# Performance work log

Hardware: AMD Instinct MI355X
Metric: run time of the kernel (lower is better)

The kernel has to match this reference:

```python
import jax, jax.numpy as jnp
import numpy as np

N = 100000        # nodes in the batched graph
E = 1_600_000     # directed edges
G = 256           # graphs in the batch
IN, H = 3, 64
EPS = 1e-5        # BatchNorm eps (eval mode: running stats, dropout off)


def setup_inputs() -> dict:
    key = jax.random.key(0)
    ks = jax.random.split(key, 40)
    inp = {}
    inp["x"] = jax.random.normal(ks[0], (N, IN), jnp.float32)
    inp["edge_index"] = jax.random.randint(ks[1], (2, E), 0, N, dtype=jnp.int32)
    inp["batch_idx"] = jnp.sort(jax.random.randint(ks[2], (N,), 0, G, dtype=jnp.int32))
    dims = [IN, H, H, H]  # zip(dims[:-1], dims[1:]) -> 3 GCN layers (as in source)
    k = 3
    for i in range(3):
        inp[f"W{i}"] = jax.random.normal(ks[k], (dims[i], dims[i + 1]), jnp.float32) * 0.1; k += 1
        inp[f"b{i}"] = jax.random.normal(ks[k], (dims[i + 1],), jnp.float32) * 0.01; k += 1
        inp[f"g{i}"] = jax.random.uniform(ks[k], (dims[i + 1],), jnp.float32, 0.5, 1.5); k += 1
        inp[f"be{i}"] = jax.random.normal(ks[k], (dims[i + 1],), jnp.float32) * 0.1; k += 1
        inp[f"rm{i}"] = jax.random.normal(ks[k], (dims[i + 1],), jnp.float32) * 0.1; k += 1
        inp[f"rv{i}"] = jax.random.uniform(ks[k], (dims[i + 1],), jnp.float32, 0.5, 1.5); k += 1
    inp["mW1"] = jax.random.normal(ks[k], (2 * H, 32), jnp.float32) * 0.1; k += 1
    inp["mb1"] = jnp.zeros((32,), jnp.float32)
    inp["mW2"] = jax.random.normal(ks[k], (32, 16), jnp.float32) * 0.1; k += 1
    inp["mb2"] = jnp.zeros((16,), jnp.float32)
    inp["mW3"] = jax.random.normal(ks[k], (16, 1), jnp.float32) * 0.1; k += 1
    inp["mb3"] = jnp.zeros((1,), jnp.float32)
    return inp


def _gcn(x, W, b, src, dst):
    # PyG GCNConv: add self-loops, symmetric D^-1/2 (A+I) D^-1/2 normalization
    h = x @ W                                   # [N, out]
    deg = jnp.zeros((N,), h.dtype).at[dst].add(1.0) + 1.0  # +1 self-loop
    dinv = jax.lax.rsqrt(deg)
    coef = dinv[src] * dinv[dst]                # [E]
    agg = jax.ops.segment_sum(h[src] * coef[:, None], dst, num_segments=N)
    agg = agg + h * (dinv * dinv)[:, None]      # self-loop message
    return agg + b


def _bn(x, g, be, rm, rv):
    return (x - rm) * jax.lax.rsqrt(rv + EPS) * g + be


def _forward(x, edge_index, batch_idx,
             W0, b0, g0, be0, rm0, rv0,
             W1, b1, g1, be1, rm1, rv1,
             W2, b2, g2, be2, rm2, rv2,
             mW1, mb1, mW2, mb2, mW3, mb3):
    src, dst = edge_index[0], edge_index[1]
    layers = [(W0, b0, g0, be0, rm0, rv0), (W1, b1, g1, be1, rm1, rv1), (W2, b2, g2, be2, rm2, rv2)]
    for (W, b, g, be, rm, rv) in layers:
        x = jax.nn.relu(_bn(_gcn(x, W, b, src, dst), g, be, rm, rv))
    cnt = jax.ops.segment_sum(jnp.ones((N,), x.dtype), batch_idx, num_segments=G)
    x_mean = jax.ops.segment_sum(x, batch_idx, num_segments=G) / jnp.maximum(cnt, 1.0)[:, None]
    x_max = jax.ops.segment_max(x, batch_idx, num_segments=G)
    x_max = jnp.where(jnp.isfinite(x_max), x_max, 0.0)
    xg = jnp.concatenate([x_mean, x_max], axis=1)  # [G, 2H]
    h = jax.nn.relu(xg @ mW1 + mb1)
    h = jax.nn.relu(h @ mW2 + mb2)
    return h @ mW3 + mb3                            # [G, 1]


def reference(x, edge_index, batch_idx,
              W0, b0, g0, be0, rm0, rv0,
              W1, b1, g1, be1, rm1, rv1,
              W2, b2, g2, be2, rm2, rv2,
              mW1, mb1, mW2, mb2, mW3, mb3):
    return _forward(x, edge_index, batch_idx,
                    W0, b0, g0, be0, rm0, rv0,
                    W1, b1, g1, be1, rm1, rv1,
                    W2, b2, g2, be2, rm2, rv2,
                    mW1, mb1, mW2, mb2, mW3, mb3)
```

## Files before the change

### kernel.cpp

```cpp
#include <hip/hip_runtime.h>
#include <hip/hip_fp16.h>

#define NN 100000
#define EE 1600000
#define GG 256
#define EPS 1e-5f
#define KB2 ((NN + 511) >> 9)
#define BCAP 10240
#define EPB 4096
#define EBLK ((EE + EPB - 1) / EPB)
#define NB256 ((NN + 255) / 256)

__device__ __forceinline__ unsigned int pack2(float x, float y) {
  __half2 h = __float22half2_rn(make_float2(x, y));
  return *reinterpret_cast<unsigned int*>(&h);
}
__device__ __forceinline__ uint2 pack4(float x, float y, float z, float w) {
  uint2 r;
  r.x = pack2(x, y);
  r.y = pack2(z, w);
  return r;
}
__device__ __forceinline__ void add8(float4& a0, float4& a1, uint4 v) {
  __half2 h0 = *reinterpret_cast<__half2*>(&v.x);
  __half2 h1 = *reinterpret_cast<__half2*>(&v.y);
  __half2 h2 = *reinterpret_cast<__half2*>(&v.z);
  __half2 h3 = *reinterpret_cast<__half2*>(&v.w);
  float2 f0 = __half22float2(h0), f1 = __half22float2(h1);
  float2 f2 = __half22float2(h2), f3 = __half22float2(h3);
  a0.x += f0.x; a0.y += f0.y; a0.z += f1.x; a0.w += f1.y;
  a1.x += f2.x; a1.y += f2.y; a1.z += f3.x; a1.w += f3.y;
}

__device__ __forceinline__ void gld16(uint4& d, const uint4* p) {
  asm volatile("global_load_dwordx4 %0, %1, off" : "=v"(d) : "v"(p));
}
__device__ __forceinline__ void gld4(int& d, const int* p) {
  asm volatile("global_load_dword %0, %1, off" : "=v"(d) : "v"(p));
}

__global__ void k_passA(const int* __restrict__ ei, int* __restrict__ bfill,
                        int* __restrict__ tmp) {
  __shared__ int cnt[KB2], cur[KB2], base[KB2];
  int t = threadIdx.x;
  for (int b = t; b < KB2; b += 256) { cnt[b] = 0; cur[b] = 0; }
  __syncthreads();
  int e0 = blockIdx.x * EPB;
  int myb[16];
#pragma unroll
  for (int j = 0; j < 16; ++j) {
    int e = e0 + j * 256 + t;
    int bb = -1;
    if (e < EE) bb = ei[EE + e] >> 9;
    myb[j] = bb;
    if (bb >= 0) atomicAdd(&cnt[bb], 1);
  }
  __syncthreads();
  for (int b = t; b < KB2; b += 256)
    if (cnt[b] > 0) base[b] = b * BCAP + atomicAdd(&bfill[b], cnt[b]);
  __syncthreads();
#pragma unroll
  for (int j = 0; j < 16; ++j) {
    int e = e0 + j * 256 + t;
    int bb = myb[j];
    if (bb >= 0) {
      int slot = base[bb] + atomicAdd(&cur[bb], 1);
      tmp[slot] = (ei[e] << 9) | (ei[EE + e] & 511);
    }
  }
}

__global__ void k_bucket(const int* __restrict__ tmp, const int* __restrict__ bfill,
                         const float* __restrict__ x, int* __restrict__ csr,
                         int* __restrict__ row, int* __restrict__ rowe,
                         float* __restrict__ dinv, float4* __restrict__ xd) {
  __shared__ int cnt[512], s[512], fillp[512];
  int b = blockIdx.x, t = threadIdx.x;
  int nb = b << 9;
  int e0 = b * BCAP, e1 = e0 + bfill[b];
  cnt[t] = 0;
  cnt[t + 256] = 0;
  __syncthreads();
  for (int e = e0 + t; e < e1; e += 256) atomicAdd(&cnt[tmp[e] & 511], 1);
  __syncthreads();
  s[t] = cnt[t];
  s[t + 256] = cnt[t + 256];
  __syncthreads();
  for (int off = 1; off < 512; off <<= 1) {
    int i1 = t + 256;
    int v0 = (t >= off) ? s[t - off] : 0;
    int v1 = (i1 >= off) ? s[i1 - off] : 0;
    __syncthreads();
    s[t] += v0;
    s[i1] += v1;
    __syncthreads();
  }
#pragma unroll
  for (int k = 0; k < 2; ++k) {
    int i = t + k * 256;
    int excl = s[i] - cnt[i];
    fillp[i] = excl;
    int dst = nb + i;
    if (dst < NN) {
      row[dst] = e0 + excl;
      rowe[dst] = e0 + s[i];
      float d = rsqrtf((float)cnt[i] + 1.0f);
      dinv[dst] = d;
      xd[dst] = make_float4(x[dst * 3] * d, x[dst * 3 + 1] * d, x[dst * 3 + 2] * d, 0.f);
    }
  }
  __syncthreads();
  for (int e = e0 + t; e < e1; e += 256) {
    int ed = tmp[e];
    int slot = atomicAdd(&fillp[ed & 511], 1);
    csr[e0 + slot] = ed >> 9;
  }
}

__global__ void k_agg3f(const float4* __restrict__ xd, const int* __restrict__ row,
                        const int* __restrict__ rowe, const int* __restrict__ csr,
                        const float* __restrict__ dinv,
                        const float* __restrict__ W, const float* __restrict__ b,
                        const float* __restrict__ gam, const float* __restrict__ bet,
                        const float* __restrict__ rm, const float* __restrict__ rv,
                        uint2* __restrict__ out) {
  int n = blockIdx.x * 256 + threadIdx.x;
  if (n >= NN) return;
  int s0 = row[n], s1 = rowe[n];
  float4 a = xd[n];
  float ax = a.x, ay = a.y, az = a.z;
  for (int i = s0; i < s1; i += 16) {
    int rem = s1 - i;
    int idx[16];
#pragma unroll
    for (int j = 0; j < 16; ++j) idx[j] = csr[min(i + j, s1 - 1)];
    float4 v[16];
#pragma unroll
    for (int j = 0; j < 16; ++j) v[j] = xd[idx[j]];
#pragma unroll
    for (int j = 0; j < 16; ++j)
      if (j < rem) { ax += v[j].x; ay += v[j].y; az += v[j].z; }
  }
  float d = dinv[n];
  float t0 = ax * d, t1 = ay * d, t2 = az * d;
  const float4* W4 = (const float4*)W;
  const float4* b4 = (const float4*)b;
  const float4* g4p = (const float4*)gam;
  const float4* be4p = (const float4*)bet;
  const float4* rm4p = (const float4*)rm;
  const float4* rv4p = (const float4*)rv;
#pragma unroll
  for (int c4 = 0; c4 < 16; ++c4) {
    float4 w0 = W4[c4], w1 = W4[16 + c4], w2 = W4[32 + c4];
    float4 bb = b4[c4], g4 = g4p[c4], be4 = be4p[c4], rm4 = rm4p[c4], rv4 = rv4p[c4];
    float4 o;
    o.x = fmaf(t0, w0.x, fmaf(t1, w1.x, fmaf(t2, w2.x, bb.x)));
    o.y = fmaf(t0, w0.y, fmaf(t1, w1.y, fmaf(t2, w2.y, bb.y)));
    o.z = fmaf(t0, w0.z, fmaf(t1, w1.z, fmaf(t2, w2.z, bb.z)));
    o.w = fmaf(t0, w0.w, fmaf(t1, w1.w, fmaf(t2, w2.w, bb.w)));
    float scx = g4.x * rsqrtf(rv4.x + EPS), shx = be4.x - rm4.x * scx;
    float scy = g4.y * rsqrtf(rv4.y + EPS), shy = be4.y - rm4.y * scy;
    float scz = g4.z * rsqrtf(rv4.z + EPS), shz = be4.z - rm4.z * scz;
    float scw = g4.w * rsqrtf(rv4.w + EPS), shw = be4.w - rm4.w * scw;
    o.x = fmaxf(fmaf(o.x, scx, shx), 0.f) * d;
    o.y = fmaxf(fmaf(o.y, scy, shy), 0.f) * d;
    o.z = fmaxf(fmaf(o.z, scz, shz), 0.f) * d;
    o.w = fmaxf(fmaf(o.w, scw, shw), 0.f) * d;
    out[(size_t)n * 16 + c4] = pack4(o.x, o.y, o.z, o.w);
  }
}

template <bool MID>
__launch_bounds__(256, 4)
__global__ void k_layer2(const uint4* __restrict__ xs, const int* __restrict__ row,
                         const int* __restrict__ rowe, const int* __restrict__ csr,
                         const float* __restrict__ dinv,
                         const float* __restrict__ W, const float* __restrict__ b,
                         const float* __restrict__ gam, const float* __restrict__ bet,
                         const float* __restrict__ rm, const float* __restrict__ rv,
                         void* __restrict__ outv) {
  __shared__ float sh[32][68];
  int t = blockIdx.x * 256 + threadIdx.x;
  int n = t >> 3, sub = t & 7;
  int local = threadIdx.x >> 3;
  int s0 = row[n], s1 = rowe[n];
  float4 a0 = make_float4(0.f, 0.f, 0.f, 0.f);
  float4 a1 = make_float4(0.f, 0.f, 0.f, 0.f);
  add8(a0, a1, xs[(size_t)n * 8 + sub]);
  if (s0 < s1) {
    int e = s0 + sub;
    int myidx = (e < s1) ? csr[e] : n;
    for (int i = s0; i < s1; i += 8) {
      int e2 = i + 8 + sub;
      int pre;
      gld4(pre, csr + min(e2, s1 - 1));
      uint4 v0, v1, v2, v3, v4, v5, v6, v7;
      gld16(v0, xs + ((size_t)__shfl(myidx, 0, 8) * 8 + sub));
      gld16(v1, xs + ((size_t)__shfl(myidx, 1, 8) * 8 + sub));
      gld16(v2, xs + ((size_t)__shfl(myidx, 2, 8) * 8 + sub));
      gld16(v3, xs + ((size_t)__shfl(myidx, 3, 8) * 8 + sub));
      gld16(v4, xs + ((size_t)__shfl(myidx, 4, 8) * 8 + sub));
      gld16(v5, xs + ((size_t)__shfl(myidx, 5, 8) * 8 + sub));
      gld16(v6, xs + ((size_t)__shfl(myidx, 6, 8) * 8 + sub));
      gld16(v7, xs + ((size_t)__shfl(myidx, 7, 8) * 8 + sub));
      asm volatile("s_waitcnt vmcnt(0)" ::: "memory");
      __builtin_amdgcn_sched_barrier(0);
      int rem = s1 - i;
      add8(a0, a1, v0);
      if (rem > 1) add8(a0, a1, v1);
      if (rem > 2) add8(a0, a1, v2);
      if (rem > 3) add8(a0, a1, v3);
      if (rem > 4) add8(a0, a1, v4);
      if (rem > 5) add8(a0, a1, v5);
      if (rem > 6) add8(a0, a1, v6);
      if (rem > 7) add8(a0, a1, v7);
      myidx = (e2 < s1) ? pre : n;
    }
  }
  float d = dinv[n];
  float4 w0 = make_float4(a0.x * d, a0.y * d, a0.z * d, a0.w * d);
  float4 w1 = make_float4(a1.x * d, a1.y * d, a1.z * d, a1.w * d);
  *(float4*)&sh[local][sub * 8] = w0;
  *(float4*)&sh[local][sub * 8 + 4] = w1;
  __syncthreads();
  const float4* W4 = (const float4*)W;
  float4 accA = ((const float4*)b)[sub * 2];
  float4 accB = ((const float4*)b)[sub * 2 + 1];
#pragma unroll 8
  for (int k = 0; k < 64; ++k) {
    float xv = sh[local][k];
    float4 wA = W4[k * 16 + sub * 2];
    float4 wB = W4[k * 16 + sub * 2 + 1];
    accA.x = fmaf(xv, wA.x, accA.x);
    accA.y = fmaf(xv, wA.y, accA.y);
    accA.z = fmaf(xv, wA.z, accA.z);
    accA.w = fmaf(xv, wA.w, accA.w);
    accB.x = fmaf(xv, wB.x, accB.x);
    accB.y = fmaf(xv, wB.y, accB.y);
    accB.z = fmaf(xv, wB.z, accB.z);
    accB.w = fmaf(xv, wB.w, accB.w);
  }
  float4 gA = ((const float4*)gam)[sub * 2], gB = ((const float4*)gam)[sub * 2 + 1];
  float4 beA = ((const float4*)bet)[sub * 2], beB = ((const float4*)bet)[sub * 2 + 1];
  float4 rmA = ((const float4*)rm)[sub * 2], rmB = ((const float4*)rm)[sub * 2 + 1];
  float4 rvA = ((const float4*)rv)[sub * 2], rvB = ((const float4*)rv)[sub * 2 + 1];
  float4 oA, oB;
  {
    float sc = gA.x * rsqrtf(rvA.x + EPS); oA.x = fmaxf(fmaf(accA.x, sc, beA.x - rmA.x * sc), 0.f);
    sc = gA.y * rsqrtf(rvA.y + EPS); oA.y = fmaxf(fmaf(accA.y, sc, beA.y - rmA.y * sc), 0.f);
    sc = gA.z * rsqrtf(rvA.z + EPS); oA.z = fmaxf(fmaf(accA.z, sc, beA.z - rmA.z * sc), 0.f);
    sc = gA.w * rsqrtf(rvA.w + EPS); oA.w = fmaxf(fmaf(accA.w, sc, beA.w - rmA.w * sc), 0.f);
    sc = gB.x * rsqrtf(rvB.x + EPS); oB.x = fmaxf(fmaf(accB.x, sc, beB.x - rmB.x * sc), 0.f);
    sc = gB.y * rsqrtf(rvB.y + EPS); oB.y = fmaxf(fmaf(accB.y, sc, beB.y - rmB.y * sc), 0.f);
    sc = gB.z * rsqrtf(rvB.z + EPS); oB.z = fmaxf(fmaf(accB.z, sc, beB.z - rmB.z * sc), 0.f);
    sc = gB.w * rsqrtf(rvB.w + EPS); oB.w = fmaxf(fmaf(accB.w, sc, beB.w - rmB.w * sc), 0.f);
  }
  if (MID) {
    uint4 r;
    r.x = pack2(oA.x * d, oA.y * d);
    r.y = pack2(oA.z * d, oA.w * d);
    r.z = pack2(oB.x * d, oB.y * d);
    r.w = pack2(oB.z * d, oB.w * d);
    ((uint4*)outv)[(size_t)n * 8 + sub] = r;
  } else {
    ((float4*)outv)[(size_t)n * 16 + sub * 2] = oA;
    ((float4*)outv)[(size_t)n * 16 + sub * 2 + 1] = oB;
  }
}

__device__ __forceinline__ int lower_bound(const int* __restrict__ b, int target) {
  int lo = 0, hi = NN;
  while (lo < hi) {
    int m = (lo + hi) >> 1;
    if (b[m] < target) lo = m + 1; else hi = m;
  }
  return lo;
}

__global__ void k_poolmlp(const float4* __restrict__ feat, const int* __restrict__ bidx,
                          const float* __restrict__ mW1, const float* __restrict__ mb1,
                          const float* __restrict__ mW2, const float* __restrict__ mb2,
                          const float* __restrict__ mW3, const float* __restrict__ mb3,
                          float* __restrict__ out) {
  __shared__ float4 shs[16][17], shm[16][17];
  __shared__ float xg[128], h1[32], h2[16];
  int g = blockIdx.x, t = threadIdx.x;
  int c4 = t & 15, r = t >> 4;
  int lo = lower_bound(bidx, g);
  int hi = lower_bound(bidx, g + 1);
  float4 s = make_float4(0.f, 0.f, 0.f, 0.f);
  float4 m = make_float4(0.f, 0.f, 0.f, 0.f);
  for (int i = lo + r; i < hi; i += 16) {
    float4 v = feat[(size_t)i * 16 + c4];
    s.x += v.x; s.y += v.y; s.z += v.z; s.w += v.w;
    m.x = fmaxf(m.x, v.x); m.y = fmaxf(m.y, v.y);
    m.z = fmaxf(m.z, v.z); m.w = fmaxf(m.w, v.w);
  }
  shs[r][c4] = s;
  shm[r][c4] = m;
  __syncthreads();
  if (t < 16) {
    float4 cs = shs[0][t], cm = shm[0][t];
#pragma unroll
    for (int r2 = 1; r2 < 16; ++r2) {
      float4 as = shs[r2][t], am = shm[r2][t];
      cs.x += as.x; cs.y += as.y; cs.z += as.z; cs.w += as.w;
      cm.x = fmaxf(cm.x, am.x); cm.y = fmaxf(cm.y, am.y);
      cm.z = fmaxf(cm.z, am.z); cm.w = fmaxf(cm.w, am.w);
    }
    float inv = 1.0f / fmaxf((float)(hi - lo), 1.0f);
    xg[t * 4 + 0] = cs.x * inv; xg[t * 4 + 1] = cs.y * inv;
    xg[t * 4 + 2] = cs.z * inv; xg[t * 4 + 3] = cs.w * inv;
    xg[64 + t * 4 + 0] = cm.x; xg[64 + t * 4 + 1] = cm.y;
    xg[64 + t * 4 + 2] = cm.z; xg[64 + t * 4 + 3] = cm.w;
  }
  __syncthreads();
  if (t < 32) {
    float a = mb1[t];
    for (int k = 0; k < 128; ++k) a = fmaf(xg[k], mW1[k * 32 + t], a);
    h1[t] = fmaxf(a, 0.f);
  }
  __syncthreads();
  if (t < 16) {
    float a = mb2[t];
    for (int k = 0; k < 32; ++k) a = fmaf(h1[k], mW2[k * 16 + t], a);
    h2[t] = fmaxf(a, 0.f);
  }
  __syncthreads();
  if (t == 0) {
    float a = mb3[0];
    for (int k = 0; k < 16; ++k) a = fmaf(h2[k], mW3[k], a);
    out[g] = a;
  }
}

extern "C" void kernel_launch(void* const* d_in, const int* in_sizes, int n_in,
                              void* d_out, int out_size, void* d_ws, size_t ws_size,
                              hipStream_t stream) {
  const float* x = (const float*)d_in[0];
  const int* ei = (const int*)d_in[1];
  const int* bidx = (const int*)d_in[2];
  const float *W[3], *b[3], *gam[3], *bet[3], *rm[3], *rv[3];
  for (int l = 0; l < 3; ++l) {
    W[l] = (const float*)d_in[3 + 6 * l];
    b[l] = (const float*)d_in[4 + 6 * l];
    gam[l] = (const float*)d_in[5 + 6 * l];
    bet[l] = (const float*)d_in[6 + 6 * l];
    rm[l] = (const float*)d_in[7 + 6 * l];
    rv[l] = (const float*)d_in[8 + 6 * l];
  }
  const float* mW1 = (const float*)d_in[21];
  const float* mb1 = (const float*)d_in[22];
  const float* mW2 = (const float*)d_in[23];
  const float* mb2 = (const float*)d_in[24];
  const float* mW3 = (const float*)d_in[25];
  const float* mb3 = (const float*)d_in[26];
  float* out = (float*)d_out;

  char* ws = (char*)d_ws;
  size_t off = 0;
  auto alloc = [&](size_t bytes) {
    void* p = ws + off;
    off = (off + bytes + 1023) & ~(size_t)1023;
    return p;
  };
  float* dinv = (float*)alloc(NN * 4);
  int* row = (int*)alloc(NN * 4);
  int* rowe = (int*)alloc(NN * 4);
  int* csr = (int*)alloc((size_t)KB2 * BCAP * 4);
  int* bfill = (int*)alloc(256 * 4);
  float4* xd = (float4*)alloc((size_t)NN * 16);
  float* bufA = (float*)alloc((size_t)NN * 64 * 4);
  float* bufB = (float*)alloc((size_t)NN * 64 * 2);
  int* tmp = (int*)bufA;

  hipMemsetAsync(bfill, 0, 256 * 4, stream);

  k_passA<<<EBLK, 256, 0, stream>>>(ei, bfill, tmp);
  k_bucket<<<KB2, 256, 0, stream>>>(tmp, bfill, x, csr, row, rowe, dinv, xd);

  int nb8 = (NN * 8) / 256;

  k_agg3f<<<NB256, 256, 0, stream>>>(xd, row, rowe, csr, dinv, W[0], b[0], gam[0], bet[0],
                                     rm[0], rv[0], (uint2*)bufA);
  k_layer2<true><<<nb8, 256, 0, stream>>>((const uint4*)bufA, row, rowe, csr, dinv, W[1], b[1],
                                          gam[1], bet[1], rm[1], rv[1], (void*)bufB);
  k_layer2<false><<<nb8, 256, 0, stream>>>((const uint4*)bufB, row, rowe, csr, dinv, W[2], b[2],
                                           gam[2], bet[2], rm[2], rv[2], (void*)bufA);
  k_poolmlp<<<GG, 256, 0, stream>>>((const float4*)bufA, bidx, mW1, mb1, mW2, mb2, mW3, mb3, out);
}
```

Baseline: 337.9 us.

## Stage bucket edges in LDS, hand-schedule gathers, widen pooling blocks

Several unrelated tweaks across the pipeline. passA keeps the packed src/dst word in registers instead of reloading edge_index in its second pass. k_bucket copies its bucket of packed edges into shared memory once instead of reading global memory twice. k_agg3f issues its index and feature gathers through inline-asm loads with explicit waitcnt and sched barriers, and gets launch bounds. The pooling kernel moves to 1024 threads with 64 row groups for more parallelism per graph. Risks: the 40KB of LDS in k_bucket lowers occupancy, and the forced full waits may serialize latency hiding.

```diff
diff --git a/kernel.cpp b/kernel.cpp
--- a/kernel.cpp
+++ b/kernel.cpp
@@ -35,6 +35,9 @@
 __device__ __forceinline__ void gld16(uint4& d, const uint4* p) {
   asm volatile("global_load_dwordx4 %0, %1, off" : "=v"(d) : "v"(p));
 }
+__device__ __forceinline__ void gldf16(float4& d, const float4* p) {
+  asm volatile("global_load_dwordx4 %0, %1, off" : "=v"(d) : "v"(p));
+}
 __device__ __forceinline__ void gld4(int& d, const int* p) {
   asm volatile("global_load_dword %0, %1, off" : "=v"(d) : "v"(p));
 }
@@ -46,13 +49,19 @@
   for (int b = t; b < KB2; b += 256) { cnt[b] = 0; cur[b] = 0; }
   __syncthreads();
   int e0 = blockIdx.x * EPB;
-  int myb[16];
+  int myb[16], myp[16];
 #pragma unroll
   for (int j = 0; j < 16; ++j) {
     int e = e0 + j * 256 + t;
-    int bb = -1;
-    if (e < EE) bb = ei[EE + e] >> 9;
+    int bb = -1, pp = 0;
+    if (e < EE) {
+      int ss = ei[e];
+      int dd = ei[EE + e];
+      bb = dd >> 9;
+      pp = (ss << 9) | (dd & 511);
+    }
     myb[j] = bb;
+    myp[j] = pp;
     if (bb >= 0) atomicAdd(&cnt[bb], 1);
   }
   __syncthreads();
@@ -61,11 +70,10 @@
   __syncthreads();
 #pragma unroll
   for (int j = 0; j < 16; ++j) {
-    int e = e0 + j * 256 + t;
     int bb = myb[j];
     if (bb >= 0) {
       int slot = base[bb] + atomicAdd(&cur[bb], 1);
-      tmp[slot] = (ei[e] << 9) | (ei[EE + e] & 511);
+      tmp[slot] = myp[j];
     }
   }
 }
@@ -75,13 +83,16 @@
                          int* __restrict__ row, int* __restrict__ rowe,
                          float* __restrict__ dinv, float4* __restrict__ xd) {
   __shared__ int cnt[512], s[512], fillp[512];
+  __shared__ int stmp[BCAP];
   int b = blockIdx.x, t = threadIdx.x;
   int nb = b << 9;
-  int e0 = b * BCAP, e1 = e0 + bfill[b];
+  int e0 = b * BCAP;
+  int fill = bfill[b];
   cnt[t] = 0;
   cnt[t + 256] = 0;
-  __syncthreads();
-  for (int e = e0 + t; e < e1; e += 256) atomicAdd(&cnt[tmp[e] & 511], 1);
+  for (int e = t; e < fill; e += 256) stmp[e] = tmp[e0 + e];
+  __syncthreads();
+  for (int e = t; e < fill; e += 256) atomicAdd(&cnt[stmp[e] & 511], 1);
   __syncthreads();
   s[t] = cnt[t];
   s[t + 256] = cnt[t + 256];
@@ -110,13 +121,14 @@
     }
   }
   __syncthreads();
-  for (int e = e0 + t; e < e1; e += 256) {
-    int ed = tmp[e];
+  for (int e = t; e < fill; e += 256) {
+    int ed = stmp[e];
     int slot = atomicAdd(&fillp[ed & 511], 1);
     csr[e0 + slot] = ed >> 9;
   }
 }
 
+__launch_bounds__(256, 4)
 __global__ void k_agg3f(const float4* __restrict__ xd, const int* __restrict__ row,
                         const int* __restrict__ rowe, const int* __restrict__ csr,
                         const float* __restrict__ dinv,
@@ -130,13 +142,17 @@
   float4 a = xd[n];
   float ax = a.x, ay = a.y, az = a.z;
   for (int i = s0; i < s1; i += 16) {
+    int idx[16];
+#pragma unroll
+    for (int j = 0; j < 16; ++j) gld4(idx[j], csr + min(i + j, s1 - 1));
+    asm volatile("s_waitcnt vmcnt(0)" ::: "memory");
+    __builtin_amdgcn_sched_barrier(0);
+    float4 v[16];
+#pragma unroll
+    for (int j = 0; j < 16; ++j) gldf16(v[j], xd + idx[j]);
+    asm volatile("s_waitcnt vmcnt(0)" ::: "memory");
+    __builtin_amdgcn_sched_barrier(0);
     int rem = s1 - i;
-    int idx[16];
-#pragma unroll
-    for (int j = 0; j < 16; ++j) idx[j] = csr[min(i + j, s1 - 1)];
-    float4 v[16];
-#pragma unroll
-    for (int j = 0; j < 16; ++j) v[j] = xd[idx[j]];
 #pragma unroll
     for (int j = 0; j < 16; ++j)
       if (j < rem) { ax += v[j].x; ay += v[j].y; az += v[j].z; }
@@ -282,7 +298,7 @@
                           const float* __restrict__ mW2, const float* __restrict__ mb2,
                           const float* __restrict__ mW3, const float* __restrict__ mb3,
                           float* __restrict__ out) {
-  __shared__ float4 shs[16][17], shm[16][17];
+  __shared__ float4 shs[64][17], shm[64][17];
   __shared__ float xg[128], h1[32], h2[16];
   int g = blockIdx.x, t = threadIdx.x;
   int c4 = t & 15, r = t >> 4;
@@ -290,7 +306,7 @@
   int hi = lower_bound(bidx, g + 1);
   float4 s = make_float4(0.f, 0.f, 0.f, 0.f);
   float4 m = make_float4(0.f, 0.f, 0.f, 0.f);
-  for (int i = lo + r; i < hi; i += 16) {
+  for (int i = lo + r; i < hi; i += 64) {
     float4 v = feat[(size_t)i * 16 + c4];
     s.x += v.x; s.y += v.y; s.z += v.z; s.w += v.w;
     m.x = fmaxf(m.x, v.x); m.y = fmaxf(m.y, v.y);
@@ -302,7 +318,7 @@
   if (t < 16) {
     float4 cs = shs[0][t], cm = shm[0][t];
 #pragma unroll
-    for (int r2 = 1; r2 < 16; ++r2) {
+    for (int r2 = 1; r2 < 64; ++r2) {
       float4 as = shs[r2][t], am = shm[r2][t];
       cs.x += as.x; cs.y += as.y; cs.z += as.z; cs.w += as.w;
       cm.x = fmaxf(cm.x, am.x); cm.y = fmaxf(cm.y, am.y);
@@ -387,5 +403,5 @@
                                           gam[1], bet[1], rm[1], rv[1], (void*)bufB);
   k_layer2<false><<<nb8, 256, 0, stream>>>((const uint4*)bufB, row, rowe, csr, dinv, W[2], b[2],
                                            gam[2], bet[2], rm[2], rv[2], (void*)bufA);
-  k_poolmlp<<<GG, 256, 0, stream>>>((const float4*)bufA, bidx, mW1, mb1, mW2, mb2, mW3, mb3, out);
-}
+  k_poolmlp<<<GG, 1024, 0, stream>>>((const float4*)bufA, bidx, mW1, mb1, mW2, mb2, mW3, mb3, out);
+}
```

Result: faster. 323.8 us (-4.2%).
